# Performance work log

Measured on AMD Instinct MI355X. Metric: run time of the kernel, lower is better.

The kernel has to match this reference:

```python
import jax, jax.numpy as jnp
import numpy as np

N_NODES = 100000
N_EDGES = 1600000
NFEAT, NHID, NCLASS = 128, 64, 16


def setup_inputs() -> dict:
    key = jax.random.key(0)
    k1, k2, k3, k4, k5 = jax.random.split(key, 5)
    x = jax.random.normal(k1, (N_NODES, NFEAT), dtype=jnp.float32)
    edge_index = jax.random.randint(k2, (2, N_EDGES), 0, N_NODES, dtype=jnp.int64)
    edge_weight = jax.random.uniform(k3, (N_EDGES,), dtype=jnp.float32)
    # PyG Linear default init ~ kaiming-uniform; plain scaled normals suffice as a baseline
    W1 = jax.random.normal(k4, (NFEAT, NHID), dtype=jnp.float32) / np.sqrt(NFEAT)
    W2 = jax.random.normal(k5, (NHID, NCLASS), dtype=jnp.float32) / np.sqrt(NHID)
    return {"x": x, "edge_index": edge_index, "edge_weight": edge_weight, "W1": W1, "W2": W2}


def _gcn_conv(x, W, src, dst, w, num_nodes):
    # GCNConv(normalize=False, add_self_loops=False, bias=False):
    # out[dst] = sum_{e: dst(e)=dst} w_e * (x @ W)[src(e)]
    h = x @ W                                    # [N, out]
    msg = w[:, None] * h[src]                    # [E, out] gathered messages
    return jax.ops.segment_sum(msg, dst, num_segments=num_nodes)


def reference(x, edge_index, edge_weight, W1, W2):
    src, dst = edge_index[0], edge_index[1]
    h = jax.nn.relu(_gcn_conv(x, W1, src, dst, edge_weight, N_NODES))
    out = _gcn_conv(h, W2, src, dst, edge_weight, N_NODES)
    return out
```

## Files before the change

kernel.cpp:

```cpp
#include <hip/hip_runtime.h>
#include <hip/hip_fp16.h>

#define N_NODES 100000
#define N_EDGES 1600000
#define NFEAT 128
#define NHID 64
#define NCLASS 16

#define NPB 98
#define NB 1024
#define HIST_EPT 16
#define HIST_BLOCKS ((N_EDGES + 256 * HIST_EPT - 1) / (256 * HIST_EPT))
#define FILL_EPT 16
#define FILL_BLOCKS ((N_EDGES + 256 * FILL_EPT - 1) / (256 * FILL_EPT))
#define NTILES ((N_NODES + 15) / 16)
#define GEMM_BLOCKS ((NTILES + 3) / 4)

typedef unsigned int u32;
typedef __attribute__((ext_vector_type(8))) _Float16 f16x8;
typedef __attribute__((ext_vector_type(4))) float f32x4;

__device__ __forceinline__ __half2 u2h2(u32 u) { __half2 h; __builtin_memcpy(&h, &u, 4); return h; }
__device__ __forceinline__ u32 h22u(__half2 h) { u32 u; __builtin_memcpy(&u, &h, 4); return u; }
__device__ __forceinline__ u32 pack_h16(float a, float b) { return h22u(__floats2half2_rn(a, b)); }

__device__ __forceinline__ int detect_i32(const void* ei) {
    u32 v = ((const u32*)ei)[2 * (threadIdx.x & 63) + 1];
    return (__ballot(v != 0) != 0ULL) ? 1 : 0;
}

__device__ __forceinline__ int load_idx(const void* ei, int flag, size_t pos) {
    return flag ? ((const int*)ei)[pos] : (int)((const long long*)ei)[pos];
}

__global__ __launch_bounds__(256) void mega1_kernel(const float* __restrict__ X,
                                                    const float* __restrict__ W,
                                                    u32* __restrict__ Y,
                                                    const void* __restrict__ ei,
                                                    int* __restrict__ ghist) {
    __shared__ float Wsh[NFEAT * NHID];
    int t = threadIdx.x;
    if (blockIdx.x < GEMM_BLOCKS) {
        for (int i = t; i < NFEAT * NHID; i += 256) Wsh[i] = W[i];
        __syncthreads();
        int wid = t >> 6;
        int lane = t & 63;
        int r = lane & 15, g = lane >> 4;
        int m0 = (blockIdx.x * 4 + wid) * 16;
        if (m0 >= N_NODES) return;

        f16x8 af[4][4];
#pragma unroll
        for (int nt = 0; nt < 4; ++nt)
#pragma unroll
            for (int kt = 0; kt < 4; ++kt)
#pragma unroll
                for (int j = 0; j < 8; ++j)
                    af[nt][kt][j] = (_Float16)Wsh[(kt * 32 + g * 8 + j) * NHID + nt * 16 + r];

        const float* xr = X + (size_t)(m0 + r) * NFEAT + g * 8;
        f16x8 bfr[4];
#pragma unroll
        for (int kt = 0; kt < 4; ++kt) {
            float4 v0 = *(const float4*)(xr + kt * 32);
            float4 v1 = *(const float4*)(xr + kt * 32 + 4);
            bfr[kt][0] = (_Float16)v0.x; bfr[kt][1] = (_Float16)v0.y;
            bfr[kt][2] = (_Float16)v0.z; bfr[kt][3] = (_Float16)v0.w;
            bfr[kt][4] = (_Float16)v1.x; bfr[kt][5] = (_Float16)v1.y;
            bfr[kt][6] = (_Float16)v1.z; bfr[kt][7] = (_Float16)v1.w;
        }

        u32* yr = Y + (size_t)(m0 + r) * (NHID / 2);
#pragma unroll
        for (int nt = 0; nt < 4; ++nt) {
            f32x4 acc = {0.f, 0.f, 0.f, 0.f};
#pragma unroll
            for (int kt = 0; kt < 4; ++kt)
                acc = __builtin_amdgcn_mfma_f32_16x16x32_f16(af[nt][kt], bfr[kt], acc, 0, 0, 0);
            uint2 o;
            o.x = pack_h16(acc[0], acc[1]);
            o.y = pack_h16(acc[2], acc[3]);
            *(uint2*)(yr + nt * 8 + g * 2) = o;
        }
    } else {
        int* cnt = (int*)Wsh;
        int bid = blockIdx.x - GEMM_BLOCKS;
#pragma unroll
        for (int k = 0; k < NB / 256; ++k) cnt[t + k * 256] = 0;
        __syncthreads();
        int f = detect_i32(ei);
        int base = bid * 256 * HIST_EPT;
#pragma unroll
        for (int k = 0; k < HIST_EPT; ++k) {
            int e = base + k * 256 + t;
            if (e < N_EDGES) {
                int d = load_idx(ei, f, (size_t)N_EDGES + e);
                atomicAdd(&cnt[d / NPB], 1);
            }
        }
        __syncthreads();
#pragma unroll
        for (int k = 0; k < NB / 256; ++k)
            if (cnt[t + k * 256] > 0) atomicAdd(&ghist[t + k * 256], cnt[t + k * 256]);
    }
}

__global__ __launch_bounds__(1024) void scanA_kernel(const int* __restrict__ ghist,
                                                     int* __restrict__ bstart,
                                                     int* __restrict__ gcursor) {
    __shared__ int lds[NB];
    int t = threadIdx.x;
    int own = ghist[t];
    lds[t] = own;
    __syncthreads();
    for (int off = 1; off < NB; off <<= 1) {
        int v = (t >= off) ? lds[t - off] : 0;
        __syncthreads();
        lds[t] += v;
        __syncthreads();
    }
    int excl = lds[t] - own;
    bstart[t] = excl;
    if (t == NB - 1) bstart[NB] = lds[NB - 1];
    gcursor[t] = excl;
}

__global__ __launch_bounds__(256) void fillA_kernel(const void* __restrict__ ei,
                                                    const float* __restrict__ ew,
                                                    int* __restrict__ gcursor,
                                                    int2* __restrict__ ebuf) {
    __shared__ int cnt[NB];
    __shared__ int base[NB];
    int t = threadIdx.x;
#pragma unroll
    for (int k = 0; k < NB / 256; ++k) cnt[t + k * 256] = 0;
    __syncthreads();
    int f = detect_i32(ei);
    int eb = blockIdx.x * 256 * FILL_EPT;
    int src[FILL_EPT], bin[FILL_EPT], rank[FILL_EPT];
    float w[FILL_EPT];
#pragma unroll
    for (int k = 0; k < FILL_EPT; ++k) {
        int e = eb + k * 256 + t;
        bin[k] = -1;
        if (e < N_EDGES) {
            int s = load_idx(ei, f, (size_t)e);
            int d = load_idx(ei, f, (size_t)N_EDGES + e);
            int b = d / NPB;
            src[k] = s | ((d - b * NPB) << 20);
            w[k] = ew[e];
            bin[k] = b;
            rank[k] = atomicAdd(&cnt[b], 1);
        }
    }
    __syncthreads();
#pragma unroll
    for (int k = 0; k < NB / 256; ++k)
        if (cnt[t + k * 256] > 0) base[t + k * 256] = atomicAdd(&gcursor[t + k * 256], cnt[t + k * 256]);
    __syncthreads();
#pragma unroll
    for (int k = 0; k < FILL_EPT; ++k) {
        if (bin[k] >= 0) {
            int pos = base[bin[k]] + rank[k];
            ebuf[pos] = make_int2(src[k], __float_as_int(w[k]));
        }
    }
}

__global__ __launch_bounds__(256) void sortB_kernel(const int2* __restrict__ ebuf,
                                                    const int* __restrict__ bstart,
                                                    int2* __restrict__ ebuf2,
                                                    int* __restrict__ row_ptr) {
    __shared__ int cnt[NPB];
    __shared__ int sc[256];
    __shared__ int cur[NPB];
    int t = threadIdx.x, b = blockIdx.x;
    if (t < NPB) cnt[t] = 0;
    __syncthreads();
    int start = bstart[b], end = bstart[b + 1];
    for (int i = start + t; i < end; i += 256) {
        int dl = ((u32)ebuf[i].x) >> 20;
        atomicAdd(&cnt[dl], 1);
    }
    __syncthreads();
    int own = (t < NPB) ? cnt[t] : 0;
    sc[t] = own;
    __syncthreads();
    for (int off = 1; off < 256; off <<= 1) {
        int v = (t >= off) ? sc[t - off] : 0;
        __syncthreads();
        sc[t] += v;
        __syncthreads();
    }
    int excl = sc[t] - own;
    if (t < NPB) {
        cur[t] = excl;
        int node = b * NPB + t;
        if (node < N_NODES) row_ptr[node] = start + excl;
    }
    if (b == 0 && t == 0) row_ptr[N_NODES] = N_EDGES;
    __syncthreads();
    for (int i = start + t; i < end; i += 256) {
        int2 p = ebuf[i];
        int dl = ((u32)p.x) >> 20;
        int pos = start + atomicAdd(&cur[dl], 1);
        ebuf2[pos] = make_int2(p.x & 0xFFFFF, p.y);
    }
}

__global__ __launch_bounds__(256) void gemm2_kernel(const u32* __restrict__ Hb,
                                                    const float* __restrict__ W,
                                                    u32* __restrict__ Y) {
    __shared__ float Wsh[NHID * NCLASS];
    int t = threadIdx.x;
    for (int i = t; i < NHID * NCLASS; i += 256) Wsh[i] = W[i];
    __syncthreads();
    int wid = t >> 6;
    int lane = t & 63;
    int r = lane & 15, g = lane >> 4;
    int m0 = (blockIdx.x * 4 + wid) * 16;
    if (m0 >= N_NODES) return;

    f16x8 af[2];
#pragma unroll
    for (int kt = 0; kt < 2; ++kt)
#pragma unroll
        for (int j = 0; j < 8; ++j)
            af[kt][j] = (_Float16)Wsh[(kt * 32 + g * 8 + j) * NCLASS + r];

    const u32* hr = Hb + (size_t)(m0 + r) * (NHID / 2) + g * 4;
    union { uint4 u; f16x8 h; } b0, b1;
    b0.u = *(const uint4*)(hr + 0);
    b1.u = *(const uint4*)(hr + 16);

    f32x4 acc = {0.f, 0.f, 0.f, 0.f};
    acc = __builtin_amdgcn_mfma_f32_16x16x32_f16(af[0], b0.h, acc, 0, 0, 0);
    acc = __builtin_amdgcn_mfma_f32_16x16x32_f16(af[1], b1.h, acc, 0, 0, 0);

    u32* yr = Y + (size_t)(m0 + r) * (NCLASS / 2);
    uint2 o;
    o.x = pack_h16(acc[0], acc[1]);
    o.y = pack_h16(acc[2], acc[3]);
    *(uint2*)(yr + g * 2) = o;
}

__global__ __launch_bounds__(256) void agg1_kernel(const u32* __restrict__ xwb,
                                                   const int* __restrict__ row_ptr,
                                                   const int2* __restrict__ ep,
                                                   u32* __restrict__ hb) {
    int t = blockIdx.x * 256 + threadIdx.x;
    int node = t >> 6;
    int lane = t & 63;
    int p = lane & 7;
    int sub = lane >> 3;
    if (node >= N_NODES) return;
    int start = row_ptr[node], end = row_ptr[node + 1];
    int last = end - 1;
    __half2 a0 = u2h2(0), a1 = u2h2(0), a2 = u2h2(0), a3 = u2h2(0);
    __half2 b0 = u2h2(0), b1 = u2h2(0), b2 = u2h2(0), b3 = u2h2(0);
    for (int i = start + sub; i < end; i += 16) {
        int j1 = min(i + 8, last);
        int2 p0 = ep[i];
        int2 p1 = ep[j1];
        uint4 u0 = *(const uint4*)(xwb + (size_t)p0.x * 32 + 4 * p);
        uint4 u1 = *(const uint4*)(xwb + (size_t)p1.x * 32 + 4 * p);
        float w0f = __int_as_float(p0.y);
        float w1f = (i + 8 < end) ? __int_as_float(p1.y) : 0.f;
        __half2 w0 = __half2half2(__float2half(w0f));
        __half2 w1 = __half2half2(__float2half(w1f));
        a0 = __hfma2(u2h2(u0.x), w0, a0); a1 = __hfma2(u2h2(u0.y), w0, a1);
        a2 = __hfma2(u2h2(u0.z), w0, a2); a3 = __hfma2(u2h2(u0.w), w0, a3);
        b0 = __hfma2(u2h2(u1.x), w1, b0); b1 = __hfma2(u2h2(u1.y), w1, b1);
        b2 = __hfma2(u2h2(u1.z), w1, b2); b3 = __hfma2(u2h2(u1.w), w1, b3);
    }
    a0 = __hadd2(a0, b0); a1 = __hadd2(a1, b1);
    a2 = __hadd2(a2, b2); a3 = __hadd2(a3, b3);
#pragma unroll
    for (int m = 8; m <= 32; m <<= 1) {
        a0 = __hadd2(a0, u2h2((u32)__shfl_xor((int)h22u(a0), m, 64)));
        a1 = __hadd2(a1, u2h2((u32)__shfl_xor((int)h22u(a1), m, 64)));
        a2 = __hadd2(a2, u2h2((u32)__shfl_xor((int)h22u(a2), m, 64)));
        a3 = __hadd2(a3, u2h2((u32)__shfl_xor((int)h22u(a3), m, 64)));
    }
    if (sub == 0) {
        float2 f0 = __half22float2(a0);
        float2 f1 = __half22float2(a1);
        float2 f2 = __half22float2(a2);
        float2 f3 = __half22float2(a3);
        uint4 o;
        o.x = pack_h16(fmaxf(f0.x, 0.f), fmaxf(f0.y, 0.f));
        o.y = pack_h16(fmaxf(f1.x, 0.f), fmaxf(f1.y, 0.f));
        o.z = pack_h16(fmaxf(f2.x, 0.f), fmaxf(f2.y, 0.f));
        o.w = pack_h16(fmaxf(f3.x, 0.f), fmaxf(f3.y, 0.f));
        *(uint4*)(hb + (size_t)node * 32 + 4 * p) = o;
    }
}

__global__ __launch_bounds__(256) void agg2_kernel(const u32* __restrict__ hwb,
                                                   const int* __restrict__ row_ptr,
                                                   const int2* __restrict__ ep,
                                                   float* __restrict__ out) {
    int t = blockIdx.x * 256 + threadIdx.x;
    int node = t >> 6;
    int lane = t & 63;
    int p = lane & 1;
    int sub = lane >> 1;
    if (node >= N_NODES) return;
    int start = row_ptr[node], end = row_ptr[node + 1];
    __half2 a0 = u2h2(0), a1 = u2h2(0), a2 = u2h2(0), a3 = u2h2(0);
    for (int i = start + sub; i < end; i += 32) {
        int2 pr = ep[i];
        uint4 u = *(const uint4*)(hwb + (size_t)pr.x * 8 + 4 * p);
        __half2 w = __half2half2(__float2half(__int_as_float(pr.y)));
        a0 = __hfma2(u2h2(u.x), w, a0); a1 = __hfma2(u2h2(u.y), w, a1);
        a2 = __hfma2(u2h2(u.z), w, a2); a3 = __hfma2(u2h2(u.w), w, a3);
    }
#pragma unroll
    for (int m = 2; m <= 32; m <<= 1) {
        a0 = __hadd2(a0, u2h2((u32)__shfl_xor((int)h22u(a0), m, 64)));
        a1 = __hadd2(a1, u2h2((u32)__shfl_xor((int)h22u(a1), m, 64)));
        a2 = __hadd2(a2, u2h2((u32)__shfl_xor((int)h22u(a2), m, 64)));
        a3 = __hadd2(a3, u2h2((u32)__shfl_xor((int)h22u(a3), m, 64)));
    }
    if (sub == 0) {
        float2 f0 = __half22float2(a0);
        float2 f1 = __half22float2(a1);
        float2 f2 = __half22float2(a2);
        float2 f3 = __half22float2(a3);
        float* op = out + (size_t)node * NCLASS + 8 * p;
        *(float4*)(op + 0) = make_float4(f0.x, f0.y, f1.x, f1.y);
        *(float4*)(op + 4) = make_float4(f2.x, f2.y, f3.x, f3.y);
    }
}

extern "C" void kernel_launch(void* const* d_in, const int* in_sizes, int n_in,
                              void* d_out, int out_size, void* d_ws, size_t ws_size,
                              hipStream_t stream) {
    const float* x  = (const float*)d_in[0];
    const void*  ei = d_in[1];
    const float* ew = (const float*)d_in[2];
    const float* W1 = (const float*)d_in[3];
    const float* W2 = (const float*)d_in[4];
    float* out = (float*)d_out;

    char* ws = (char*)d_ws;
    size_t off = 0;
    auto take = [&](size_t bytes) {
        char* p = ws + off;
        off += (bytes + 511) & ~(size_t)511;
        return p;
    };
    int*   ghist   = (int*)take(NB * 4);
    int*   bstart  = (int*)take((NB + 1) * 4);
    int*   gcursor = (int*)take(NB * 4);
    int*   row_ptr = (int*)take((size_t)(N_NODES + 1) * 4);
    int2*  ebuf    = (int2*)take((size_t)N_EDGES * 8);
    int2*  ebuf2   = (int2*)take((size_t)N_EDGES * 8);
    u32*   xwb     = (u32*)take((size_t)N_NODES * (NHID / 2) * 4);
    u32*   hb      = (u32*)take((size_t)N_NODES * (NHID / 2) * 4);
    u32*   hwb     = (u32*)take((size_t)N_NODES * (NCLASS / 2) * 4);

    hipMemsetAsync(ghist, 0, NB * 4, stream);
    mega1_kernel<<<GEMM_BLOCKS + HIST_BLOCKS, 256, 0, stream>>>(x, W1, xwb, ei, ghist);
    scanA_kernel<<<1, NB, 0, stream>>>(ghist, bstart, gcursor);
    fillA_kernel<<<FILL_BLOCKS, 256, 0, stream>>>(ei, ew, gcursor, ebuf);
    sortB_kernel<<<NB, 256, 0, stream>>>(ebuf, bstart, ebuf2, row_ptr);

    agg1_kernel<<<(N_NODES * 64 + 255) / 256, 256, 0, stream>>>(xwb, row_ptr, ebuf2, hb);
    gemm2_kernel<<<GEMM_BLOCKS, 256, 0, stream>>>(hb, W2, hwb);
    agg2_kernel<<<(N_NODES * 64 + 255) / 256, 256, 0, stream>>>(hwb, row_ptr, ebuf2, out);
}
```

Before: 139.4 us.

## Fuse second-layer GEMM into first aggregation epilogue and replace memset

The second-layer matmul (H @ W2) now runs inside the first aggregation kernel's epilogue. Each lane multiplies its ReLU'd partial features by W2 columns it keeps in registers, and a shuffle reduction then writes the fp16 hwb row directly. This removes the gemm2 launch and the write and reread of the 64-wide hidden buffer. The hipMemsetAsync is also swapped for a tiny zeroing kernel. In exchange, every wave loads 16 W2 values per lane, and the projection now uses fp32 FMA instead of fp16 MFMA on fp16-rounded hidden values, which shifts the numerics slightly.

```diff
diff --git a/kernel.cpp b/kernel.cpp
--- a/kernel.cpp
+++ b/kernel.cpp
@@ -31,6 +31,12 @@
 
 __device__ __forceinline__ int load_idx(const void* ei, int flag, size_t pos) {
     return flag ? ((const int*)ei)[pos] : (int)((const long long*)ei)[pos];
+}
+
+__global__ __launch_bounds__(256) void zeroA_kernel(int* __restrict__ ghist) {
+    int t = threadIdx.x;
+#pragma unroll
+    for (int k = 0; k < NB / 256; ++k) ghist[t + k * 256] = 0;
 }
 
 __global__ __launch_bounds__(256) void mega1_kernel(const float* __restrict__ X,
@@ -208,52 +214,23 @@
     }
 }
 
-__global__ __launch_bounds__(256) void gemm2_kernel(const u32* __restrict__ Hb,
-                                                    const float* __restrict__ W,
-                                                    u32* __restrict__ Y) {
-    __shared__ float Wsh[NHID * NCLASS];
-    int t = threadIdx.x;
-    for (int i = t; i < NHID * NCLASS; i += 256) Wsh[i] = W[i];
-    __syncthreads();
-    int wid = t >> 6;
-    int lane = t & 63;
-    int r = lane & 15, g = lane >> 4;
-    int m0 = (blockIdx.x * 4 + wid) * 16;
-    if (m0 >= N_NODES) return;
-
-    f16x8 af[2];
-#pragma unroll
-    for (int kt = 0; kt < 2; ++kt)
-#pragma unroll
-        for (int j = 0; j < 8; ++j)
-            af[kt][j] = (_Float16)Wsh[(kt * 32 + g * 8 + j) * NCLASS + r];
-
-    const u32* hr = Hb + (size_t)(m0 + r) * (NHID / 2) + g * 4;
-    union { uint4 u; f16x8 h; } b0, b1;
-    b0.u = *(const uint4*)(hr + 0);
-    b1.u = *(const uint4*)(hr + 16);
-
-    f32x4 acc = {0.f, 0.f, 0.f, 0.f};
-    acc = __builtin_amdgcn_mfma_f32_16x16x32_f16(af[0], b0.h, acc, 0, 0, 0);
-    acc = __builtin_amdgcn_mfma_f32_16x16x32_f16(af[1], b1.h, acc, 0, 0, 0);
-
-    u32* yr = Y + (size_t)(m0 + r) * (NCLASS / 2);
-    uint2 o;
-    o.x = pack_h16(acc[0], acc[1]);
-    o.y = pack_h16(acc[2], acc[3]);
-    *(uint2*)(yr + g * 2) = o;
-}
-
-__global__ __launch_bounds__(256) void agg1_kernel(const u32* __restrict__ xwb,
-                                                   const int* __restrict__ row_ptr,
-                                                   const int2* __restrict__ ep,
-                                                   u32* __restrict__ hb) {
+__global__ __launch_bounds__(256) void agg1f_kernel(const u32* __restrict__ xwb,
+                                                    const int* __restrict__ row_ptr,
+                                                    const int2* __restrict__ ep,
+                                                    const float* __restrict__ W2,
+                                                    u32* __restrict__ hwb) {
     int t = blockIdx.x * 256 + threadIdx.x;
     int node = t >> 6;
     int lane = t & 63;
     int p = lane & 7;
     int sub = lane >> 3;
     if (node >= N_NODES) return;
+    float w2a[8], w2b[8];
+#pragma unroll
+    for (int j = 0; j < 8; ++j) {
+        w2a[j] = W2[(8 * p + j) * NCLASS + 2 * sub];
+        w2b[j] = W2[(8 * p + j) * NCLASS + 2 * sub + 1];
+    }
     int start = row_ptr[node], end = row_ptr[node + 1];
     int last = end - 1;
     __half2 a0 = u2h2(0), a1 = u2h2(0), a2 = u2h2(0), a3 = u2h2(0);
@@ -282,18 +259,24 @@
         a2 = __hadd2(a2, u2h2((u32)__shfl_xor((int)h22u(a2), m, 64)));
         a3 = __hadd2(a3, u2h2((u32)__shfl_xor((int)h22u(a3), m, 64)));
     }
-    if (sub == 0) {
-        float2 f0 = __half22float2(a0);
-        float2 f1 = __half22float2(a1);
-        float2 f2 = __half22float2(a2);
-        float2 f3 = __half22float2(a3);
-        uint4 o;
-        o.x = pack_h16(fmaxf(f0.x, 0.f), fmaxf(f0.y, 0.f));
-        o.y = pack_h16(fmaxf(f1.x, 0.f), fmaxf(f1.y, 0.f));
-        o.z = pack_h16(fmaxf(f2.x, 0.f), fmaxf(f2.y, 0.f));
-        o.w = pack_h16(fmaxf(f3.x, 0.f), fmaxf(f3.y, 0.f));
-        *(uint4*)(hb + (size_t)node * 32 + 4 * p) = o;
-    }
+    float2 f0 = __half22float2(a0);
+    float2 f1 = __half22float2(a1);
+    float2 f2 = __half22float2(a2);
+    float2 f3 = __half22float2(a3);
+    float h0 = fmaxf(f0.x, 0.f), h1 = fmaxf(f0.y, 0.f);
+    float h2 = fmaxf(f1.x, 0.f), h3 = fmaxf(f1.y, 0.f);
+    float h4 = fmaxf(f2.x, 0.f), h5 = fmaxf(f2.y, 0.f);
+    float h6 = fmaxf(f3.x, 0.f), h7 = fmaxf(f3.y, 0.f);
+    float po0 = h0 * w2a[0] + h1 * w2a[1] + h2 * w2a[2] + h3 * w2a[3]
+              + h4 * w2a[4] + h5 * w2a[5] + h6 * w2a[6] + h7 * w2a[7];
+    float po1 = h0 * w2b[0] + h1 * w2b[1] + h2 * w2b[2] + h3 * w2b[3]
+              + h4 * w2b[4] + h5 * w2b[5] + h6 * w2b[6] + h7 * w2b[7];
+#pragma unroll
+    for (int m = 1; m <= 4; m <<= 1) {
+        po0 += __shfl_xor(po0, m, 64);
+        po1 += __shfl_xor(po1, m, 64);
+    }
+    if (p == 0) hwb[(size_t)node * 8 + sub] = pack_h16(po0, po1);
 }
 
 __global__ __launch_bounds__(256) void agg2_kernel(const u32* __restrict__ hwb,
@@ -357,16 +340,14 @@
     int2*  ebuf    = (int2*)take((size_t)N_EDGES * 8);
     int2*  ebuf2   = (int2*)take((size_t)N_EDGES * 8);
     u32*   xwb     = (u32*)take((size_t)N_NODES * (NHID / 2) * 4);
-    u32*   hb      = (u32*)take((size_t)N_NODES * (NHID / 2) * 4);
     u32*   hwb     = (u32*)take((size_t)N_NODES * (NCLASS / 2) * 4);
 
-    hipMemsetAsync(ghist, 0, NB * 4, stream);
+    zeroA_kernel<<<1, 256, 0, stream>>>(ghist);
     mega1_kernel<<<GEMM_BLOCKS + HIST_BLOCKS, 256, 0, stream>>>(x, W1, xwb, ei, ghist);
     scanA_kernel<<<1, NB, 0, stream>>>(ghist, bstart, gcursor);
     fillA_kernel<<<FILL_BLOCKS, 256, 0, stream>>>(ei, ew, gcursor, ebuf);
     sortB_kernel<<<NB, 256, 0, stream>>>(ebuf, bstart, ebuf2, row_ptr);
 
-    agg1_kernel<<<(N_NODES * 64 + 255) / 256, 256, 0, stream>>>(xwb, row_ptr, ebuf2, hb);
-    gemm2_kernel<<<GEMM_BLOCKS, 256, 0, stream>>>(hb, W2, hwb);
+    agg1f_kernel<<<(N_NODES * 64 + 255) / 256, 256, 0, stream>>>(xwb, row_ptr, ebuf2, W2, hwb);
     agg2_kernel<<<(N_NODES * 64 + 255) / 256, 256, 0, stream>>>(hwb, row_ptr, ebuf2, out);
 }
```

After: 208.3 us. 49.4% more time.
